# Performance work log

Measured on AMD Instinct MI355X. Metric: run time of the kernel, lower is better.

The kernel has to match this reference:

```python
import jax, jax.numpy as jnp
import numpy as np

N = 16777216

def setup_inputs() -> dict:
    key = jax.random.key(0)
    kx, kl, kh = jax.random.split(key, 3)
    x = jax.random.normal(kx, (N,), dtype=jnp.float32)
    low = jax.random.normal(kl, (N,), dtype=jnp.float32)
    high = jax.random.normal(kh, (N,), dtype=jnp.float32)
    return {"x": x, "low": low, "high": high}

def reference(x, low, high):
    # DeepPoly ReLU relaxation. The torch code builds diagonal weight matrices;
    # the math is purely elementwise: out = slope * bound + intercept.
    crossing = (low < 0) & (high > 0)          # unstable neuron
    inactive = high <= 0                        # always-off neuron
    safe_denom = jnp.where(crossing, high - low, jnp.float32(1.0))
    # Upper bound: crossing -> chord; inactive -> 0; active -> identity.
    ub_slope = jnp.where(crossing, high / safe_denom,
                         jnp.where(inactive, 0.0, 1.0))
    ub_int = jnp.where(crossing, -(low * high) / safe_denom, 0.0)
    # Lower bound slope: crossing -> minimum-area lambda (0 if low^2 > high^2 else 1);
    # inactive -> 0; active -> identity.
    lamda = jnp.where(low * low > high * high, 0.0, 1.0).astype(x.dtype)
    lb_slope = jnp.where(crossing, lamda, jnp.where(inactive, 0.0, 1.0))
    x_out = jax.nn.relu(x)
    high_out = ub_slope * high + ub_int
    low_out = lb_slope * low                    # bias_low is zero
    return (x_out, low_out, high_out)
```

## Files before the change

kernel.cpp:

```cpp
#include <hip/hip_runtime.h>


typedef float f32x4 __attribute__((ext_vector_type(4)));

__device__ __forceinline__ void relax1(float x, float l, float h,
                                       float& xo, float& lo, float& ho) {
    bool crossing = (l < 0.0f) && (h > 0.0f);
    bool inactive = (h <= 0.0f);
    float inv = __builtin_amdgcn_rcpf(h - l);
    float ub_slope = crossing ? (h * inv) : (inactive ? 0.0f : 1.0f);
    float ub_int   = crossing ? (-(l * h) * inv) : 0.0f;
    float lamda    = (l * l > h * h) ? 0.0f : 1.0f;
    float lb_slope = crossing ? lamda : (inactive ? 0.0f : 1.0f);
    xo = fmaxf(x, 0.0f);
    ho = ub_slope * h + ub_int;
    lo = lb_slope * l;
}

__device__ __forceinline__ void relax4(f32x4 xv, f32x4 lv, f32x4 hv,
                                       f32x4& xr, f32x4& lr, f32x4& hr) {
#pragma unroll
    for (int j = 0; j < 4; ++j) {
        float xo, lo, ho;
        relax1(xv[j], lv[j], hv[j], xo, lo, ho);
        xr[j] = xo;
        lr[j] = lo;
        hr[j] = ho;
    }
}

__global__ __launch_bounds__(256) void abstract_relu_kernel(
        const f32x4* __restrict__ x,
        const f32x4* __restrict__ low,
        const f32x4* __restrict__ high,
        f32x4* __restrict__ x_out,
        f32x4* __restrict__ low_out,
        f32x4* __restrict__ high_out) {
    int base = blockIdx.x * 512 + threadIdx.x;
    int i0 = base;
    int i1 = base + 256;

    f32x4 xv0 = __builtin_nontemporal_load(&x[i0]);
    f32x4 lv0 = __builtin_nontemporal_load(&low[i0]);
    f32x4 hv0 = __builtin_nontemporal_load(&high[i0]);
    f32x4 xv1 = __builtin_nontemporal_load(&x[i1]);
    f32x4 lv1 = __builtin_nontemporal_load(&low[i1]);
    f32x4 hv1 = __builtin_nontemporal_load(&high[i1]);

    f32x4 xr0, lr0, hr0, xr1, lr1, hr1;
    relax4(xv0, lv0, hv0, xr0, lr0, hr0);
    relax4(xv1, lv1, hv1, xr1, lr1, hr1);

    __builtin_nontemporal_store(xr0, &x_out[i0]);
    __builtin_nontemporal_store(lr0, &low_out[i0]);
    __builtin_nontemporal_store(hr0, &high_out[i0]);
    __builtin_nontemporal_store(xr1, &x_out[i1]);
    __builtin_nontemporal_store(lr1, &low_out[i1]);
    __builtin_nontemporal_store(hr1, &high_out[i1]);
}

extern "C" void kernel_launch(void* const* d_in, const int* in_sizes, int n_in,
                              void* d_out, int out_size, void* d_ws, size_t ws_size,
                              hipStream_t stream) {
    const int n = in_sizes[0];
    const int n4 = n / 4;

    const f32x4* x    = (const f32x4*)d_in[0];
    const f32x4* low  = (const f32x4*)d_in[1];
    const f32x4* high = (const f32x4*)d_in[2];

    float* out = (float*)d_out;
    f32x4* x_out    = (f32x4*)(out);
    f32x4* low_out  = (f32x4*)(out + (size_t)n);
    f32x4* high_out = (f32x4*)(out + (size_t)2 * n);

    const int block = 256;
    const int grid  = n4 / 512;
    abstract_relu_kernel<<<grid, block, 0, stream>>>(
        x, low, high, x_out, low_out, high_out);
}
```

Before: 323.3 us.

## Use persistent grid-stride loop with software-prefetched loads

```diff
diff --git a/kernel.cpp b/kernel.cpp
--- a/kernel.cpp
+++ b/kernel.cpp
@@ -3,26 +3,21 @@
 
 typedef float f32x4 __attribute__((ext_vector_type(4)));
 
-__device__ __forceinline__ void relax1(float x, float l, float h,
-                                       float& xo, float& lo, float& ho) {
-    bool crossing = (l < 0.0f) && (h > 0.0f);
-    bool inactive = (h <= 0.0f);
-    float inv = __builtin_amdgcn_rcpf(h - l);
-    float ub_slope = crossing ? (h * inv) : (inactive ? 0.0f : 1.0f);
-    float ub_int   = crossing ? (-(l * h) * inv) : 0.0f;
-    float lamda    = (l * l > h * h) ? 0.0f : 1.0f;
-    float lb_slope = crossing ? lamda : (inactive ? 0.0f : 1.0f);
-    xo = fmaxf(x, 0.0f);
-    ho = ub_slope * h + ub_int;
-    lo = lb_slope * l;
-}
-
 __device__ __forceinline__ void relax4(f32x4 xv, f32x4 lv, f32x4 hv,
                                        f32x4& xr, f32x4& lr, f32x4& hr) {
 #pragma unroll
     for (int j = 0; j < 4; ++j) {
-        float xo, lo, ho;
-        relax1(xv[j], lv[j], hv[j], xo, lo, ho);
+        float xx = xv[j], l = lv[j], h = hv[j];
+        bool crossing = (l < 0.0f) && (h > 0.0f);
+        bool inactive = (h <= 0.0f);
+        float inv = __builtin_amdgcn_rcpf(h - l);
+        float ub_slope = crossing ? (h * inv) : (inactive ? 0.0f : 1.0f);
+        float ub_int   = crossing ? (-(l * h) * inv) : 0.0f;
+        float lamda    = (l * l > h * h) ? 0.0f : 1.0f;
+        float lb_slope = crossing ? lamda : (inactive ? 0.0f : 1.0f);
+        float xo = fmaxf(xx, 0.0f);
+        float ho = ub_slope * h + ub_int;
+        float lo = lb_slope * l;
         xr[j] = xo;
         lr[j] = lo;
         hr[j] = ho;
@@ -35,28 +30,35 @@
         const f32x4* __restrict__ high,
         f32x4* __restrict__ x_out,
         f32x4* __restrict__ low_out,
-        f32x4* __restrict__ high_out) {
-    int base = blockIdx.x * 512 + threadIdx.x;
-    int i0 = base;
-    int i1 = base + 256;
+        f32x4* __restrict__ high_out,
+        int stride,
+        int iters) {
+    int i = blockIdx.x * blockDim.x + threadIdx.x;
 
-    f32x4 xv0 = __builtin_nontemporal_load(&x[i0]);
-    f32x4 lv0 = __builtin_nontemporal_load(&low[i0]);
-    f32x4 hv0 = __builtin_nontemporal_load(&high[i0]);
-    f32x4 xv1 = __builtin_nontemporal_load(&x[i1]);
-    f32x4 lv1 = __builtin_nontemporal_load(&low[i1]);
-    f32x4 hv1 = __builtin_nontemporal_load(&high[i1]);
+    f32x4 cx = __builtin_nontemporal_load(&x[i]);
+    f32x4 cl = __builtin_nontemporal_load(&low[i]);
+    f32x4 ch = __builtin_nontemporal_load(&high[i]);
 
-    f32x4 xr0, lr0, hr0, xr1, lr1, hr1;
-    relax4(xv0, lv0, hv0, xr0, lr0, hr0);
-    relax4(xv1, lv1, hv1, xr1, lr1, hr1);
+    for (int it = 1; it < iters; ++it) {
+        int ni = i + stride;
+        f32x4 nx = __builtin_nontemporal_load(&x[ni]);
+        f32x4 nl = __builtin_nontemporal_load(&low[ni]);
+        f32x4 nh = __builtin_nontemporal_load(&high[ni]);
 
-    __builtin_nontemporal_store(xr0, &x_out[i0]);
-    __builtin_nontemporal_store(lr0, &low_out[i0]);
-    __builtin_nontemporal_store(hr0, &high_out[i0]);
-    __builtin_nontemporal_store(xr1, &x_out[i1]);
-    __builtin_nontemporal_store(lr1, &low_out[i1]);
-    __builtin_nontemporal_store(hr1, &high_out[i1]);
+        f32x4 xr, lr, hr;
+        relax4(cx, cl, ch, xr, lr, hr);
+        __builtin_nontemporal_store(xr, &x_out[i]);
+        __builtin_nontemporal_store(lr, &low_out[i]);
+        __builtin_nontemporal_store(hr, &high_out[i]);
+
+        cx = nx; cl = nl; ch = nh; i = ni;
+    }
+
+    f32x4 xr, lr, hr;
+    relax4(cx, cl, ch, xr, lr, hr);
+    __builtin_nontemporal_store(xr, &x_out[i]);
+    __builtin_nontemporal_store(lr, &low_out[i]);
+    __builtin_nontemporal_store(hr, &high_out[i]);
 }
 
 extern "C" void kernel_launch(void* const* d_in, const int* in_sizes, int n_in,
@@ -74,8 +76,11 @@
     f32x4* low_out  = (f32x4*)(out + (size_t)n);
     f32x4* high_out = (f32x4*)(out + (size_t)2 * n);
 
-    const int block = 256;
-    const int grid  = n4 / 512;
+    const int block  = 256;
+    const int grid   = 2048;
+    const int stride = grid * block;
+    const int iters  = n4 / stride;
+
     abstract_relu_kernel<<<grid, block, 0, stream>>>(
-        x, low, high, x_out, low_out, high_out);
+        x, low, high, x_out, low_out, high_out, stride, iters);
 }
```

Result: no change. 323.4 us (+0.0%).

## Split relu and bound relaxation into separate block groups with grid-stride loops

Applied to the files above, without the earlier changes.

```diff
diff --git a/kernel.cpp b/kernel.cpp
--- a/kernel.cpp
+++ b/kernel.cpp
@@ -2,32 +2,6 @@
 
 
 typedef float f32x4 __attribute__((ext_vector_type(4)));
-
-__device__ __forceinline__ void relax1(float x, float l, float h,
-                                       float& xo, float& lo, float& ho) {
-    bool crossing = (l < 0.0f) && (h > 0.0f);
-    bool inactive = (h <= 0.0f);
-    float inv = __builtin_amdgcn_rcpf(h - l);
-    float ub_slope = crossing ? (h * inv) : (inactive ? 0.0f : 1.0f);
-    float ub_int   = crossing ? (-(l * h) * inv) : 0.0f;
-    float lamda    = (l * l > h * h) ? 0.0f : 1.0f;
-    float lb_slope = crossing ? lamda : (inactive ? 0.0f : 1.0f);
-    xo = fmaxf(x, 0.0f);
-    ho = ub_slope * h + ub_int;
-    lo = lb_slope * l;
-}
-
-__device__ __forceinline__ void relax4(f32x4 xv, f32x4 lv, f32x4 hv,
-                                       f32x4& xr, f32x4& lr, f32x4& hr) {
-#pragma unroll
-    for (int j = 0; j < 4; ++j) {
-        float xo, lo, ho;
-        relax1(xv[j], lv[j], hv[j], xo, lo, ho);
-        xr[j] = xo;
-        lr[j] = lo;
-        hr[j] = ho;
-    }
-}
 
 __global__ __launch_bounds__(256) void abstract_relu_kernel(
         const f32x4* __restrict__ x,
@@ -36,34 +10,54 @@
         f32x4* __restrict__ x_out,
         f32x4* __restrict__ low_out,
         f32x4* __restrict__ high_out) {
-    int base = blockIdx.x * 512 + threadIdx.x;
-    int i0 = base;
-    int i1 = base + 256;
+    const int bid = blockIdx.x;
 
-    f32x4 xv0 = __builtin_nontemporal_load(&x[i0]);
-    f32x4 lv0 = __builtin_nontemporal_load(&low[i0]);
-    f32x4 hv0 = __builtin_nontemporal_load(&high[i0]);
-    f32x4 xv1 = __builtin_nontemporal_load(&x[i1]);
-    f32x4 lv1 = __builtin_nontemporal_load(&low[i1]);
-    f32x4 hv1 = __builtin_nontemporal_load(&high[i1]);
-
-    f32x4 xr0, lr0, hr0, xr1, lr1, hr1;
-    relax4(xv0, lv0, hv0, xr0, lr0, hr0);
-    relax4(xv1, lv1, hv1, xr1, lr1, hr1);
-
-    __builtin_nontemporal_store(xr0, &x_out[i0]);
-    __builtin_nontemporal_store(lr0, &low_out[i0]);
-    __builtin_nontemporal_store(hr0, &high_out[i0]);
-    __builtin_nontemporal_store(xr1, &x_out[i1]);
-    __builtin_nontemporal_store(lr1, &low_out[i1]);
-    __builtin_nontemporal_store(hr1, &high_out[i1]);
+    if (bid < 1024) {
+        int i = bid * 256 + threadIdx.x;
+        const int stride = 1024 * 256;
+#pragma unroll
+        for (int it = 0; it < 16; ++it) {
+            f32x4 xv = __builtin_nontemporal_load(&x[i]);
+            f32x4 xr;
+            xr[0] = fmaxf(xv[0], 0.0f);
+            xr[1] = fmaxf(xv[1], 0.0f);
+            xr[2] = fmaxf(xv[2], 0.0f);
+            xr[3] = fmaxf(xv[3], 0.0f);
+            __builtin_nontemporal_store(xr, &x_out[i]);
+            i += stride;
+        }
+    } else {
+        int i = (bid - 1024) * 256 + threadIdx.x;
+        const int stride = 2048 * 256;
+#pragma unroll
+        for (int it = 0; it < 8; ++it) {
+            f32x4 lv = __builtin_nontemporal_load(&low[i]);
+            f32x4 hv = __builtin_nontemporal_load(&high[i]);
+            f32x4 lr, hr;
+#pragma unroll
+            for (int j = 0; j < 4; ++j) {
+                float l = lv[j], h = hv[j];
+                bool crossing = (l < 0.0f) && (h > 0.0f);
+                bool inactive = (h <= 0.0f);
+                float inv = __builtin_amdgcn_rcpf(h - l);
+                float ub_slope = crossing ? (h * inv) : (inactive ? 0.0f : 1.0f);
+                float ub_int   = crossing ? (-(l * h) * inv) : 0.0f;
+                float lamda    = (l * l > h * h) ? 0.0f : 1.0f;
+                float lb_slope = crossing ? lamda : (inactive ? 0.0f : 1.0f);
+                lr[j] = lb_slope * l;
+                hr[j] = ub_slope * h + ub_int;
+            }
+            __builtin_nontemporal_store(lr, &low_out[i]);
+            __builtin_nontemporal_store(hr, &high_out[i]);
+            i += stride;
+        }
+    }
 }
 
 extern "C" void kernel_launch(void* const* d_in, const int* in_sizes, int n_in,
                               void* d_out, int out_size, void* d_ws, size_t ws_size,
                               hipStream_t stream) {
     const int n = in_sizes[0];
-    const int n4 = n / 4;
 
     const f32x4* x    = (const f32x4*)d_in[0];
     const f32x4* low  = (const f32x4*)d_in[1];
@@ -75,7 +69,7 @@
     f32x4* high_out = (f32x4*)(out + (size_t)2 * n);
 
     const int block = 256;
-    const int grid  = n4 / 512;
+    const int grid  = 3072;
     abstract_relu_kernel<<<grid, block, 0, stream>>>(
         x, low, high, x_out, low_out, high_out);
 }
```

New measurement: 326.5 us. No clear change (+1.0%).
